# Kernel optimization log

Measured on AMD Instinct MI355X. Metric: run time of the kernel, lower is better.

Reference implementation:

```python
import jax, jax.numpy as jnp
from jax import lax
import numpy as np

B, INP, WIDTH, OUTP, E, H = 32, 1024, 256, 1024, 8, 14
EPS = 1e-5


def setup_inputs() -> dict:
    key = jax.random.key(0)
    ks = jax.random.split(key, 12)
    n = lambda k, s, sc=0.05: jax.random.normal(k, s, jnp.float32) * sc
    return {
        "x": jax.random.normal(ks[0], (B, INP, H, H), jnp.float32),
        "w1": n(ks[1], (E, WIDTH, INP, 1, 1)),
        "w2": n(ks[2], (E, WIDTH, WIDTH, 3, 3)),
        "w3": n(ks[3], (E, OUTP, WIDTH, 1, 1)),
        "r1_w": n(ks[4], (INP, E)), "r1_b": jnp.zeros((E,), jnp.float32),
        "r2_w": n(ks[5], (WIDTH, E)), "r2_b": jnp.zeros((E,), jnp.float32),
        "r3_w": n(ks[6], (WIDTH, E)), "r3_b": jnp.zeros((E,), jnp.float32),
        "bn1_g": jax.random.uniform(ks[7], (WIDTH,), jnp.float32, 0.5, 1.5),
        "bn1_b": n(ks[8], (WIDTH,), 0.1),
        "bn1_m": jnp.zeros((WIDTH,), jnp.float32), "bn1_v": jnp.ones((WIDTH,), jnp.float32),
        "bn2_g": jax.random.uniform(ks[9], (WIDTH,), jnp.float32, 0.5, 1.5),
        "bn2_b": n(ks[10], (WIDTH,), 0.1),
        "bn2_m": jnp.zeros((WIDTH,), jnp.float32), "bn2_v": jnp.ones((WIDTH,), jnp.float32),
        "bn3_g": jax.random.uniform(ks[11], (OUTP,), jnp.float32, 0.5, 1.5),
        "bn3_b": jnp.zeros((OUTP,), jnp.float32),
        "bn3_m": jnp.zeros((OUTP,), jnp.float32), "bn3_v": jnp.ones((OUTP,), jnp.float32),
    }


def _route(x, w, b):
    # global avg pool -> linear -> sigmoid : [B, E]
    return jax.nn.sigmoid(x.mean(axis=(2, 3)) @ w + b)


def _cond_conv(x, w, rw, stride=1, padding=0, dilation=1, groups=1):
    # x: [B,Cin,H,W]; w: [E,Cout,Cin/groups,kh,kw]; rw: [B,E]
    Bn, Cin, Hh, Ww = x.shape
    _, Cout, Cin_g, kh, kw = w.shape
    # per-sample expert-combined kernels, then batch-grouped conv
    cw = jnp.einsum('be,eoikl->boikl', rw, w).reshape(Bn * Cout, Cin_g, kh, kw)
    out = lax.conv_general_dilated(
        x.reshape(1, Bn * Cin, Hh, Ww), cw,
        window_strides=(stride, stride),
        padding=[(padding, padding), (padding, padding)],
        rhs_dilation=(dilation, dilation),
        feature_group_count=Bn * groups,
        dimension_numbers=('NCHW', 'OIHW', 'NCHW'))
    return out.reshape(Bn, Cout, out.shape[2], out.shape[3])


def _bn(x, g, b, m, v):
    inv = lax.rsqrt(v + EPS) * g
    return x * inv[None, :, None, None] + (b - m * inv)[None, :, None, None]


def reference(x, w1, w2, w3, r1_w, r1_b, r2_w, r2_b, r3_w, r3_b,
              bn1_g, bn1_b, bn1_m, bn1_v, bn2_g, bn2_b, bn2_m, bn2_v,
              bn3_g, bn3_b, bn3_m, bn3_v):
    identity = x
    rw1 = _route(x, r1_w, r1_b)
    out = jax.nn.relu(_bn(_cond_conv(x, w1, rw1), bn1_g, bn1_b, bn1_m, bn1_v))
    rw2 = _route(out, r2_w, r2_b)
    out = jax.nn.relu(_bn(_cond_conv(out, w2, rw2, stride=1, padding=1), bn2_g, bn2_b, bn2_m, bn2_v))
    rw3 = _route(out, r3_w, r3_b)
    out = _bn(_cond_conv(out, w3, rw3), bn3_g, bn3_b, bn3_m, bn3_v)
    return jax.nn.relu(out + identity)
```

## Files before the change

### kernel.cpp

```cpp
#include <hip/hip_runtime.h>
#include <hip/hip_bf16.h>

#define BB 32
#define INP 1024
#define WIDTH 256
#define OUTP 1024
#define NE 8
#define HW 196
#define HH 14
#define EPS 1e-5f

#define S1 (WIDTH * INP)
#define S2 (WIDTH * WIDTH * 9)
#define S3 (OUTP * WIDTH)

typedef __attribute__((ext_vector_type(8))) short bf16x8;
typedef __attribute__((ext_vector_type(4))) float f32x4;
typedef __attribute__((ext_vector_type(8))) unsigned short u16x8;


__device__ __forceinline__ unsigned short f2bf_bits(float f) {
    unsigned u = __float_as_uint(f);
    u += 0x7FFFu + ((u >> 16) & 1u);
    return (unsigned short)(u >> 16);
}

#if defined(__has_builtin)
#if __has_builtin(__builtin_amdgcn_global_load_lds)
#define HAVE_GLL 1
#endif
#endif
__device__ __forceinline__ void gl2lds(const unsigned short* g, unsigned short* l,
                                       int lane) {
#ifdef HAVE_GLL
    __builtin_amdgcn_global_load_lds(
        (const __attribute__((address_space(1))) unsigned int*)(const void*)g,
        (__attribute__((address_space(3))) unsigned int*)(void*)l, 16, 0, 0);
#else
    *(u16x8*)(l + lane * 8) = *(const u16x8*)g;
#endif
}

__global__ __launch_bounds__(256) void transpose_mean_x(
    const float* __restrict__ x, unsigned short* __restrict__ xb,
    float* __restrict__ mean1) {
    __shared__ float lt[128][17];
    int b = blockIdx.x, c0 = blockIdx.y * 128;
    int t = threadIdx.x, cr = t >> 1, half = t & 1;
    const float* src = x + ((size_t)(b * INP + c0 + cr)) * HW;
    float msum = 0.f;
    int j = t >> 4, nl = t & 15;
    for (int pg = 0; pg < 14; pg++) {
        int p0 = pg * 16 + half * 8;
        float vv[8];
        if (pg < 12) {
            float4 a = *(const float4*)(src + p0);
            float4 c = *(const float4*)(src + p0 + 4);
            vv[0] = a.x; vv[1] = a.y; vv[2] = a.z; vv[3] = a.w;
            vv[4] = c.x; vv[5] = c.y; vv[6] = c.z; vv[7] = c.w;
        } else {
#pragma unroll
            for (int i = 0; i < 8; i++) {
                int p = p0 + i;
                vv[i] = (p < HW) ? src[p] : 0.f;
            }
        }
#pragma unroll
        for (int i = 0; i < 8; i++) { msum += vv[i]; lt[cr][half * 8 + i] = vv[i]; }
        __syncthreads();
        unsigned short pk[8];
#pragma unroll
        for (int i = 0; i < 8; i++) pk[i] = f2bf_bits(lt[j * 8 + i][nl]);
        size_t tile = ((size_t)b * 14 + pg) * 32 + (size_t)(blockIdx.y * 4 + (j >> 2));
        int lane = nl | ((j & 3) << 4);
        *(u16x8*)(xb + tile * 512 + lane * 8) = *(u16x8*)pk;
        __syncthreads();
    }
    float other = __shfl_xor(msum, 1, 64);
    if (half == 0) mean1[b * INP + c0 + cr] = (msum + other) * (1.0f / (float)HW);
}

__global__ __launch_bounds__(256) void route_kernel(const float* __restrict__ mean,
                                                    const float* __restrict__ W,
                                                    const float* __restrict__ bias,
                                                    float* __restrict__ rw, int C,
                                                    float scale) {
    __shared__ float red[NE * 256];
    int b = blockIdx.x, t = threadIdx.x;
    float part[NE];
#pragma unroll
    for (int e = 0; e < NE; e++) part[e] = 0.f;
    for (int c = t; c < C; c += 256) {
        float m = mean[b * C + c];
#pragma unroll
        for (int e = 0; e < NE; e++) part[e] += m * W[c * NE + e];
    }
#pragma unroll
    for (int e = 0; e < NE; e++) red[e * 256 + t] = part[e];
    __syncthreads();
    for (int st = 128; st > 0; st >>= 1) {
        if (t < st) {
#pragma unroll
            for (int e = 0; e < NE; e++) red[e * 256 + t] += red[e * 256 + t + st];
        }
        __syncthreads();
    }
    if (t < NE) {
        float z = red[t * 256] * scale + bias[t];
        rw[b * NE + t] = 1.0f / (1.0f + expf(-z));
    }
}

__global__ __launch_bounds__(256) void combine_cont(
    const float* __restrict__ w, const float* __restrict__ rw,
    unsigned short* __restrict__ cw, int S, int Mt, int Kt) {
    __shared__ float srw[64];
    int tid = threadIdx.x, wv = tid >> 6, lane = tid & 63, ml = lane & 15, k8l = lane >> 4;
    int g = blockIdx.y;
    if (tid < 64) srw[tid] = rw[g * 64 + tid];
    __syncthreads();
    int kq = Kt >> 2;
    int mt = blockIdx.x / kq, kt = (blockIdx.x - mt * kq) * 4 + wv;
    int K = Kt * 32;
    const float* src = w + (size_t)(mt * 16 + ml) * K + kt * 32 + k8l * 8;
    float v[NE][8];
#pragma unroll
    for (int e = 0; e < NE; e++) {
        float4 a = *(const float4*)(src + (size_t)e * S);
        float4 c = *(const float4*)(src + (size_t)e * S + 4);
        v[e][0] = a.x; v[e][1] = a.y; v[e][2] = a.z; v[e][3] = a.w;
        v[e][4] = c.x; v[e][5] = c.y; v[e][6] = c.z; v[e][7] = c.w;
    }
    size_t dto = ((size_t)mt * Kt + kt) * 512 + (size_t)lane * 8;
    size_t bstr = (size_t)Mt * Kt * 512;
    for (int bl = 0; bl < 8; bl++) {
        int b = g * 8 + bl;
        float acc[8];
#pragma unroll
        for (int jj = 0; jj < 8; jj++) acc[jj] = 0.f;
#pragma unroll
        for (int e = 0; e < NE; e++) {
            float r = srw[bl * NE + e];
#pragma unroll
            for (int jj = 0; jj < 8; jj++) acc[jj] += r * v[e][jj];
        }
        u16x8 o;
#pragma unroll
        for (int jj = 0; jj < 8; jj++) o[jj] = f2bf_bits(acc[jj]);
        *(u16x8*)(cw + (size_t)b * bstr + dto) = o;
    }
}

__global__ __launch_bounds__(256) void permute_w2(
    const float* __restrict__ w2, unsigned short* __restrict__ wb2) {
    __shared__ unsigned short lds[9 * 256];
    int eo = blockIdx.x, t = threadIdx.x;
    const float* src = w2 + (size_t)eo * 2304 + (size_t)t * 9;
#pragma unroll
    for (int t9 = 0; t9 < 9; t9++) lds[t9 * 256 + t] = f2bf_bits(src[t9]);
    __syncthreads();
    unsigned short* dst = wb2 + (size_t)eo * 2304;
    for (int j = t; j < 288; j += 256)
        *(u16x8*)(dst + j * 8) = *(const u16x8*)(lds + j * 8);
}

__global__ __launch_bounds__(256) void combine_w2(
    const unsigned short* __restrict__ wb2, const float* __restrict__ rw,
    unsigned short* __restrict__ cw) {
    __shared__ float srw[64];
    int tid = threadIdx.x, wv = tid >> 6, lane = tid & 63, ol = lane & 15, g4 = lane >> 4;
    int g = blockIdx.y;
    if (tid < 64) srw[tid] = rw[g * 64 + tid];
    __syncthreads();
    int ot = blockIdx.x / 18, kt = (blockIdx.x - ot * 18) * 4 + wv;
    const unsigned short* src = wb2 + (size_t)(ot * 16 + ol) * 2304 + kt * 32 + g4 * 8;
    float v[NE][8];
#pragma unroll
    for (int e = 0; e < NE; e++) {
        u16x8 raw = *(const u16x8*)(src + (size_t)e * S2);
#pragma unroll
        for (int jj = 0; jj < 8; jj++)
            v[e][jj] = __uint_as_float((unsigned)raw[jj] << 16);
    }
    size_t dto = ((size_t)ot * 72 + kt) * 512 + (size_t)lane * 8;
    for (int bl = 0; bl < 8; bl++) {
        int b = g * 8 + bl;
        float acc[8];
#pragma unroll
        for (int jj = 0; jj < 8; jj++) acc[jj] = 0.f;
#pragma unroll
        for (int e = 0; e < NE; e++) {
            float r = srw[bl * NE + e];
#pragma unroll
            for (int jj = 0; jj < 8; jj++) acc[jj] += r * v[e][jj];
        }
        u16x8 out;
#pragma unroll
        for (int jj = 0; jj < 8; jj++) out[jj] = f2bf_bits(acc[jj]);
        *(u16x8*)(cw + (size_t)b * (16 * 72 * 512) + dto) = out;
    }
}

__device__ __forceinline__ void stage_step(
    const unsigned short* Ab, const unsigned short* Bb, int Ktot, int kt,
    unsigned short* lA, unsigned short* lB, int wv, int lane) {
    gl2lds(Ab + ((size_t)wv * Ktot + kt) * 512 + lane * 8, lA + wv * 512, lane);
    gl2lds(Ab + ((size_t)(wv + 4) * Ktot + kt) * 512 + lane * 8, lA + (wv + 4) * 512, lane);
    gl2lds(Bb + ((size_t)wv * Ktot + kt) * 512 + lane * 8, lB + wv * 512, lane);
    if (wv < 3)
        gl2lds(Bb + ((size_t)(4 + wv) * Ktot + kt) * 512 + lane * 8, lB + (4 + wv) * 512, lane);
}

__device__ __forceinline__ void compute_step(
    const unsigned short* lA, const unsigned short* lB,
    f32x4* acc0, f32x4* acc1, int wv, int lane) {
    bf16x8 a0 = *(const bf16x8*)(lA + wv * 512 + lane * 8);
    bf16x8 a1 = *(const bf16x8*)(lA + (wv + 4) * 512 + lane * 8);
#pragma unroll
    for (int t = 0; t < 7; t++) {
        bf16x8 bt = *(const bf16x8*)(lB + t * 512 + lane * 8);
        acc0[t] = __builtin_amdgcn_mfma_f32_16x16x32_bf16(a0, bt, acc0[t], 0, 0, 0);
        acc1[t] = __builtin_amdgcn_mfma_f32_16x16x32_bf16(a1, bt, acc1[t], 0, 0, 0);
    }
}

__global__ __launch_bounds__(256) void gemm_split(
    const unsigned short* __restrict__ Bsw, const unsigned short* __restrict__ Asw,
    float* __restrict__ P, int Ktot, int ksteps) {
    __shared__ __align__(16) unsigned short lAb[4][8 * 512];
    __shared__ __align__(16) unsigned short lBb[4][7 * 512];
    int b = blockIdx.x, mh = blockIdx.y >> 1, nh = blockIdx.y & 1, s = blockIdx.z;
    int tid = threadIdx.x, wv = tid >> 6, lane = tid & 63;
    int kbase = s * ksteps;
    const unsigned short* Ab = Asw + (size_t)(b * 16 + mh * 8) * Ktot * 512;
    const unsigned short* Bb = Bsw + (size_t)(b * 14 + nh * 7) * Ktot * 512;
    f32x4 acc0[7], acc1[7];
#pragma unroll
    for (int t = 0; t < 7; t++) { acc0[t] = {0.f, 0.f, 0.f, 0.f}; acc1[t] = {0.f, 0.f, 0.f, 0.f}; }

    stage_step(Ab, Bb, Ktot, kbase + 0, lAb[0], lBb[0], wv, lane);
    stage_step(Ab, Bb, Ktot, kbase + 1, lAb[1], lBb[1], wv, lane);
    int npair = ksteps >> 1;
    for (int kp = 0; kp < npair; kp++) {
        int cb = (kp & 1) << 1, sb = 2 - cb;
        __syncthreads();
        if (kp + 1 < npair) {
            stage_step(Ab, Bb, Ktot, kbase + 2 * kp + 2, lAb[sb], lBb[sb], wv, lane);
            stage_step(Ab, Bb, Ktot, kbase + 2 * kp + 3, lAb[sb + 1], lBb[sb + 1], wv, lane);
        }
        compute_step(lAb[cb], lBb[cb], acc0, acc1, wv, lane);
        compute_step(lAb[cb + 1], lBb[cb + 1], acc0, acc1, wv, lane);
    }
#pragma unroll
    for (int a = 0; a < 2; a++) {
        int mt = mh * 8 + wv + 4 * a;
#pragma unroll
        for (int t = 0; t < 7; t++) {
            f32x4 v = a ? acc1[t] : acc0[t];
            *(f32x4*)(P + ((((size_t)s * BB + b) * 16 + mt) * 14 + nh * 7 + t) * 256 + lane * 4) = v;
        }
    }
}

__global__ __launch_bounds__(256) void gemm2_split(
    const unsigned short* __restrict__ act, const unsigned short* __restrict__ cw2,
    const unsigned short* __restrict__ zpad, float* __restrict__ P) {
    __shared__ __align__(16) unsigned short lAb[4][8 * 512];
    __shared__ __align__(16) unsigned short lBb[4][7 * 512];
    int b = blockIdx.x, mh = blockIdx.y >> 1, nh = blockIdx.y & 1, s = blockIdx.z;
    int tid = threadIdx.x, wv = tid >> 6, lane = tid & 63, lo = lane & 15, g4 = lane >> 4;
    const unsigned short* Ab = cw2 + (size_t)(b * 16 + mh * 8) * 72 * 512;
    const unsigned short* actb = act + (size_t)b * 14 * 8 * 512;

    int p0 = (nh * 7 + wv) * 16 + lo;
    int py0 = p0 / HH, px0 = p0 - (p0 / HH) * HH;
    bool pv0 = p0 < HW;
    int p1 = (nh * 7 + wv + 4) * 16 + lo;
    int py1 = p1 / HH, px1 = p1 - (p1 / HH) * HH;
    bool pv1 = (wv < 3) && (p1 < HW);

    f32x4 acc0[7], acc1[7];
#pragma unroll
    for (int t = 0; t < 7; t++) { acc0[t] = {0.f, 0.f, 0.f, 0.f}; acc1[t] = {0.f, 0.f, 0.f, 0.f}; }

    int kbase = s * 18;
    auto stage2 = [&](int kt, unsigned short* lA, unsigned short* lB) {
        gl2lds(Ab + ((size_t)wv * 72 + kt) * 512 + lane * 8, lA + wv * 512, lane);
        gl2lds(Ab + ((size_t)(wv + 4) * 72 + kt) * 512 + lane * 8, lA + (wv + 4) * 512, lane);
        int t9 = kt >> 3;
        int dy = t9 / 3 - 1, dx = t9 - (t9 / 3) * 3 - 1;
        int itile = kt & 7;
        {
            int sy = py0 + dy, sx = px0 + dx;
            bool ok = pv0 && sy >= 0 && sy < HH && sx >= 0 && sx < HH;
            int ns = sy * HH + sx;
            const unsigned short* gp = ok
                ? actb + ((size_t)(ns >> 4) * 8 + itile) * 512 + (size_t)((ns & 15) | (g4 << 4)) * 8
                : zpad;
            gl2lds(gp, lB + wv * 512, lane);
        }
        if (wv < 3) {
            int sy = py1 + dy, sx = px1 + dx;
            bool ok = pv1 && sy >= 0 && sy < HH && sx >= 0 && sx < HH;
            int ns = sy * HH + sx;
            const unsigned short* gp = ok
                ? actb + ((size_t)(ns >> 4) * 8 + itile) * 512 + (size_t)((ns & 15) | (g4 << 4)) * 8
                : zpad;
            gl2lds(gp, lB + (wv + 4) * 512, lane);
        }
    };

    stage2(kbase + 0, lAb[0], lBb[0]);
    stage2(kbase + 1, lAb[1], lBb[1]);
    for (int kp = 0; kp < 9; kp++) {
        int cb = (kp & 1) << 1, sb = 2 - cb;
        __syncthreads();
        if (kp < 8) {
            stage2(kbase + 2 * kp + 2, lAb[sb], lBb[sb]);
            stage2(kbase + 2 * kp + 3, lAb[sb + 1], lBb[sb + 1]);
        }
        compute_step(lAb[cb], lBb[cb], acc0, acc1, wv, lane);
        compute_step(lAb[cb + 1], lBb[cb + 1], acc0, acc1, wv, lane);
    }
#pragma unroll
    for (int a = 0; a < 2; a++) {
        int mt = mh * 8 + wv + 4 * a;
#pragma unroll
        for (int t = 0; t < 7; t++) {
            f32x4 v = a ? acc1[t] : acc0[t];
            *(f32x4*)(P + ((((size_t)s * BB + b) * 16 + mt) * 14 + nh * 7 + t) * 256 + lane * 4) = v;
        }
    }
}

__global__ __launch_bounds__(256) void ep12(
    const float* __restrict__ P, int S,
    const float* __restrict__ g, const float* __restrict__ be,
    const float* __restrict__ mu, const float* __restrict__ var,
    unsigned short* __restrict__ actout, float* __restrict__ msum) {
    int b = blockIdx.x;
    int tid = threadIdx.x, wv = tid >> 6, lane = tid & 63, lo = lane & 15, g4 = lane >> 4;
    int mt = blockIdx.y * 4 + wv;
    int nt0 = blockIdx.z * 7;
    int c0 = mt * 16 + g4 * 4;
    float sc[4], sh[4];
#pragma unroll
    for (int r = 0; r < 4; r++) {
        float iv = rsqrtf(var[c0 + r] + EPS) * g[c0 + r];
        sc[r] = iv;
        sh[r] = be[c0 + r] - mu[c0 + r] * iv;
    }
    const float* Pb = P + (((size_t)b * 16 + mt) * 14) * 256 + lane * 4;
    size_t pstr = (size_t)BB * 16 * 14 * 256;
    float ms[4] = {0.f, 0.f, 0.f, 0.f};
    int ktc = mt >> 1;
    int lanehi = ((mt * 2 + (g4 >> 1)) & 3) << 4;
    for (int nt = nt0; nt < nt0 + 7; nt++) {
        float v[4] = {0.f, 0.f, 0.f, 0.f};
        for (int s = 0; s < S; s++) {
            f32x4 pv = *(const f32x4*)(Pb + (size_t)s * pstr + (size_t)nt * 256);
#pragma unroll
            for (int r = 0; r < 4; r++) v[r] += pv[r];
        }
        int n = nt * 16 + lo;
#pragma unroll
        for (int r = 0; r < 4; r++) {
            float val = v[r] * sc[r] + sh[r];
            val = fmaxf(val, 0.f);
            if (n >= HW) val = 0.f;
            v[r] = val;
            ms[r] += val;
        }
        unsigned p01 = (unsigned)f2bf_bits(v[0]) | ((unsigned)f2bf_bits(v[1]) << 16);
        unsigned p23 = (unsigned)f2bf_bits(v[2]) | ((unsigned)f2bf_bits(v[3]) << 16);
        size_t off = (((size_t)(b * 14 + nt)) * 8 + ktc) * 512 + (size_t)(lo | lanehi) * 8 + (g4 & 1) * 4;
        *(uint2*)(actout + off) = make_uint2(p01, p23);
    }
#pragma unroll
    for (int r = 0; r < 4; r++) {
        float s = ms[r];
        s += __shfl_xor(s, 1, 64);
        s += __shfl_xor(s, 2, 64);
        s += __shfl_xor(s, 4, 64);
        s += __shfl_xor(s, 8, 64);
        if (lo == 0) atomicAdd(&msum[b * 256 + c0 + r], s);
    }
}

__global__ __launch_bounds__(256) void gemm3_fused(
    const unsigned short* __restrict__ Bsw, const unsigned short* __restrict__ Asw,
    const float* __restrict__ g, const float* __restrict__ be,
    const float* __restrict__ mu, const float* __restrict__ var,
    const float* __restrict__ resid, float* __restrict__ out) {
    __shared__ __align__(16) unsigned short lAb[4][8 * 512];
    __shared__ __align__(16) unsigned short lBb[4][7 * 512];
    int b = blockIdx.x, y = blockIdx.y, mh = y >> 1, nh = y & 1;
    int tid = threadIdx.x, wv = tid >> 6, lane = tid & 63, lo = lane & 15, g4 = lane >> 4;
    const unsigned short* Ab = Asw + (size_t)(b * 64 + mh * 8) * 8 * 512;
    const unsigned short* Bb = Bsw + (size_t)(b * 14 + nh * 7) * 8 * 512;
    f32x4 acc0[7], acc1[7];
#pragma unroll
    for (int t = 0; t < 7; t++) { acc0[t] = {0.f, 0.f, 0.f, 0.f}; acc1[t] = {0.f, 0.f, 0.f, 0.f}; }

    stage_step(Ab, Bb, 8, 0, lAb[0], lBb[0], wv, lane);
    stage_step(Ab, Bb, 8, 1, lAb[1], lBb[1], wv, lane);
#pragma unroll
    for (int kp = 0; kp < 4; kp++) {
        int cb = (kp & 1) << 1, sb = 2 - cb;
        __syncthreads();
        if (kp + 1 < 4) {
            stage_step(Ab, Bb, 8, 2 * kp + 2, lAb[sb], lBb[sb], wv, lane);
            stage_step(Ab, Bb, 8, 2 * kp + 3, lAb[sb + 1], lBb[sb + 1], wv, lane);
        }
        compute_step(lAb[cb], lBb[cb], acc0, acc1, wv, lane);
        compute_step(lAb[cb + 1], lBb[cb + 1], acc0, acc1, wv, lane);
    }
#pragma unroll
    for (int a = 0; a < 2; a++) {
        int mt = mh * 8 + wv + 4 * a;
        int c0 = mt * 16 + g4 * 4;
        float sc[4], sh[4];
#pragma unroll
        for (int r = 0; r < 4; r++) {
            float iv = rsqrtf(var[c0 + r] + EPS) * g[c0 + r];
            sc[r] = iv;
            sh[r] = be[c0 + r] - mu[c0 + r] * iv;
        }
#pragma unroll
        for (int t = 0; t < 7; t++) {
            int n = (nh * 7 + t) * 16 + lo;
            if (n >= HW) continue;
            f32x4 av = a ? acc1[t] : acc0[t];
#pragma unroll
            for (int r = 0; r < 4; r++) {
                size_t oidx = ((size_t)(b * OUTP + c0 + r)) * HW + n;
                float val = av[r] * sc[r] + sh[r] + resid[oidx];
                out[oidx] = fmaxf(val, 0.f);
            }
        }
    }
}

extern "C" void kernel_launch(void* const* d_in, const int* in_sizes, int n_in,
                              void* d_out, int out_size, void* d_ws, size_t ws_size,
                              hipStream_t stream) {
    const float* x    = (const float*)d_in[0];
    const float* w1   = (const float*)d_in[1];
    const float* w2   = (const float*)d_in[2];
    const float* w3   = (const float*)d_in[3];
    const float* r1_w = (const float*)d_in[4];
    const float* r1_b = (const float*)d_in[5];
    const float* r2_w = (const float*)d_in[6];
    const float* r2_b = (const float*)d_in[7];
    const float* r3_w = (const float*)d_in[8];
    const float* r3_b = (const float*)d_in[9];
    const float* bn1_g = (const float*)d_in[10];
    const float* bn1_b = (const float*)d_in[11];
    const float* bn1_m = (const float*)d_in[12];
    const float* bn1_v = (const float*)d_in[13];
    const float* bn2_g = (const float*)d_in[14];
    const float* bn2_b = (const float*)d_in[15];
    const float* bn2_m = (const float*)d_in[16];
    const float* bn2_v = (const float*)d_in[17];
    const float* bn3_g = (const float*)d_in[18];
    const float* bn3_b = (const float*)d_in[19];
    const float* bn3_m = (const float*)d_in[20];
    const float* bn3_v = (const float*)d_in[21];
    float* out = (float*)d_out;

    char* ws = (char*)d_ws;
    size_t off = 0;
    float* mean1 = (float*)(ws + off); off += (size_t)BB * INP * 4;
    float* msum2 = (float*)(ws + off); off += (size_t)BB * 256 * 4;
    float* msum3 = (float*)(ws + off); off += (size_t)BB * 256 * 4;
    float* rw1 = (float*)(ws + off); off += BB * NE * 4;
    float* rw2 = (float*)(ws + off); off += BB * NE * 4;
    float* rw3 = (float*)(ws + off); off += BB * NE * 4;
    unsigned short* zpad = (unsigned short*)(ws + off); off += 256;
    off = (off + 255) & ~(size_t)255;
    unsigned short* act = (unsigned short*)(ws + off); off += (size_t)BB * 14 * 8 * 512 * 2;
    char* cw2slot = ws + off; off += (size_t)BB * 16 * 72 * 512 * 2;
    float* P1           = (float*)cw2slot;
    unsigned short* cw2 = (unsigned short*)cw2slot;
    char* regionA = ws + off; off += (size_t)BB * (14 + 16) * 32 * 512 * 2;
    unsigned short* xb  = (unsigned short*)regionA;
    unsigned short* cw1 = (unsigned short*)(regionA + (size_t)BB * 14 * 32 * 512 * 2);
    unsigned short* wb2 = (unsigned short*)regionA;
    float* P2           = (float*)regionA;
    unsigned short* cw3 = (unsigned short*)regionA;
    (void)ws_size;

    hipMemsetAsync(zpad, 0, 256, stream);
    hipMemsetAsync(msum2, 0, (size_t)2 * BB * 256 * 4, stream);
    transpose_mean_x<<<dim3(BB, 8), 256, 0, stream>>>(x, xb, mean1);

    route_kernel<<<BB, 256, 0, stream>>>(mean1, r1_w, r1_b, rw1, INP, 1.0f);
    combine_cont<<<dim3(128, 4), 256, 0, stream>>>(w1, rw1, cw1, S1, 16, 32);
    gemm_split<<<dim3(BB, 4, 4), 256, 0, stream>>>(xb, cw1, P1, 32, 8);
    permute_w2<<<2048, 256, 0, stream>>>(w2, wb2);
    ep12<<<dim3(BB, 4, 2), 256, 0, stream>>>(P1, 4, bn1_g, bn1_b, bn1_m, bn1_v, act, msum2);

    route_kernel<<<BB, 256, 0, stream>>>(msum2, r2_w, r2_b, rw2, WIDTH, 1.0f / (float)HW);
    combine_w2<<<dim3(288, 4), 256, 0, stream>>>(wb2, rw2, cw2);
    gemm2_split<<<dim3(BB, 4, 4), 256, 0, stream>>>(act, cw2, zpad, P2);
    ep12<<<dim3(BB, 4, 2), 256, 0, stream>>>(P2, 4, bn2_g, bn2_b, bn2_m, bn2_v, act, msum3);

    route_kernel<<<BB, 256, 0, stream>>>(msum3, r3_w, r3_b, rw3, WIDTH, 1.0f / (float)HW);
    combine_cont<<<dim3(128, 4), 256, 0, stream>>>(w3, rw3, cw3, S3, 64, 8);
    gemm3_fused<<<dim3(BB, 16), 256, 0, stream>>>(act, cw3, bn3_g, bn3_b, bn3_m, bn3_v, x, out);
}
```

Baseline: 261.4 us.

## Fuse routing into combine kernels and replace split-K GEMMs with fused epilogues

```diff
diff --git a/kernel.cpp b/kernel.cpp
--- a/kernel.cpp
+++ b/kernel.cpp
@@ -39,6 +39,43 @@
 #else
     *(u16x8*)(l + lane * 8) = *(const u16x8*)g;
 #endif
+}
+
+__device__ __forceinline__ void block_route(
+    const float* __restrict__ vec, const float* __restrict__ W,
+    const float* __restrict__ bias, float scale, int C, int g,
+    float* srw, int tid) {
+    int wv = tid >> 6, lane = tid & 63;
+    float p0[NE], p1[NE];
+#pragma unroll
+    for (int e = 0; e < NE; e++) { p0[e] = 0.f; p1[e] = 0.f; }
+    const float* v0 = vec + (size_t)(g * 8 + wv * 2) * C;
+    const float* v1 = v0 + C;
+    for (int c = lane; c < C; c += 64) {
+        float4 wa = *(const float4*)(W + c * 8);
+        float4 wb = *(const float4*)(W + c * 8 + 4);
+        float m0 = v0[c], m1 = v1[c];
+        p0[0] += m0 * wa.x; p0[1] += m0 * wa.y; p0[2] += m0 * wa.z; p0[3] += m0 * wa.w;
+        p0[4] += m0 * wb.x; p0[5] += m0 * wb.y; p0[6] += m0 * wb.z; p0[7] += m0 * wb.w;
+        p1[0] += m1 * wa.x; p1[1] += m1 * wa.y; p1[2] += m1 * wa.z; p1[3] += m1 * wa.w;
+        p1[4] += m1 * wb.x; p1[5] += m1 * wb.y; p1[6] += m1 * wb.z; p1[7] += m1 * wb.w;
+    }
+#pragma unroll
+    for (int j = 1; j < 64; j <<= 1) {
+#pragma unroll
+        for (int e = 0; e < NE; e++) {
+            p0[e] += __shfl_xor(p0[e], j, 64);
+            p1[e] += __shfl_xor(p1[e], j, 64);
+        }
+    }
+    if (lane == 0) {
+#pragma unroll
+        for (int e = 0; e < NE; e++) {
+            srw[(wv * 2) * 8 + e] = 1.0f / (1.0f + expf(-(scale * p0[e] + bias[e])));
+            srw[(wv * 2 + 1) * 8 + e] = 1.0f / (1.0f + expf(-(scale * p1[e] + bias[e])));
+        }
+    }
+    __syncthreads();
 }
 
 __global__ __launch_bounds__(256) void transpose_mean_x(
@@ -80,45 +117,14 @@
     if (half == 0) mean1[b * INP + c0 + cr] = (msum + other) * (1.0f / (float)HW);
 }
 
-__global__ __launch_bounds__(256) void route_kernel(const float* __restrict__ mean,
-                                                    const float* __restrict__ W,
-                                                    const float* __restrict__ bias,
-                                                    float* __restrict__ rw, int C,
-                                                    float scale) {
-    __shared__ float red[NE * 256];
-    int b = blockIdx.x, t = threadIdx.x;
-    float part[NE];
-#pragma unroll
-    for (int e = 0; e < NE; e++) part[e] = 0.f;
-    for (int c = t; c < C; c += 256) {
-        float m = mean[b * C + c];
-#pragma unroll
-        for (int e = 0; e < NE; e++) part[e] += m * W[c * NE + e];
-    }
-#pragma unroll
-    for (int e = 0; e < NE; e++) red[e * 256 + t] = part[e];
-    __syncthreads();
-    for (int st = 128; st > 0; st >>= 1) {
-        if (t < st) {
-#pragma unroll
-            for (int e = 0; e < NE; e++) red[e * 256 + t] += red[e * 256 + t + st];
-        }
-        __syncthreads();
-    }
-    if (t < NE) {
-        float z = red[t * 256] * scale + bias[t];
-        rw[b * NE + t] = 1.0f / (1.0f + expf(-z));
-    }
-}
-
-__global__ __launch_bounds__(256) void combine_cont(
-    const float* __restrict__ w, const float* __restrict__ rw,
+__global__ __launch_bounds__(256) void combine_cont_r(
+    const float* __restrict__ w, const float* __restrict__ vec,
+    const float* __restrict__ rW, const float* __restrict__ rB, float scale, int C,
     unsigned short* __restrict__ cw, int S, int Mt, int Kt) {
     __shared__ float srw[64];
     int tid = threadIdx.x, wv = tid >> 6, lane = tid & 63, ml = lane & 15, k8l = lane >> 4;
     int g = blockIdx.y;
-    if (tid < 64) srw[tid] = rw[g * 64 + tid];
-    __syncthreads();
+    block_route(vec, rW, rB, scale, C, g, srw, tid);
     int kq = Kt >> 2;
     int mt = blockIdx.x / kq, kt = (blockIdx.x - mt * kq) * 4 + wv;
     int K = Kt * 32;
@@ -164,14 +170,14 @@
         *(u16x8*)(dst + j * 8) = *(const u16x8*)(lds + j * 8);
 }
 
-__global__ __launch_bounds__(256) void combine_w2(
-    const unsigned short* __restrict__ wb2, const float* __restrict__ rw,
+__global__ __launch_bounds__(256) void combine_w2_r(
+    const unsigned short* __restrict__ wb2, const float* __restrict__ vec,
+    const float* __restrict__ rW, const float* __restrict__ rB, float scale,
     unsigned short* __restrict__ cw) {
     __shared__ float srw[64];
     int tid = threadIdx.x, wv = tid >> 6, lane = tid & 63, ol = lane & 15, g4 = lane >> 4;
     int g = blockIdx.y;
-    if (tid < 64) srw[tid] = rw[g * 64 + tid];
-    __syncthreads();
+    block_route(vec, rW, rB, scale, 256, g, srw, tid);
     int ot = blockIdx.x / 18, kt = (blockIdx.x - ot * 18) * 4 + wv;
     const unsigned short* src = wb2 + (size_t)(ot * 16 + ol) * 2304 + kt * 32 + g4 * 8;
     float v[NE][8];
@@ -201,75 +207,108 @@
     }
 }
 
-__device__ __forceinline__ void stage_step(
-    const unsigned short* Ab, const unsigned short* Bb, int Ktot, int kt,
-    unsigned short* lA, unsigned short* lB, int wv, int lane) {
-    gl2lds(Ab + ((size_t)wv * Ktot + kt) * 512 + lane * 8, lA + wv * 512, lane);
-    gl2lds(Ab + ((size_t)(wv + 4) * Ktot + kt) * 512 + lane * 8, lA + (wv + 4) * 512, lane);
-    gl2lds(Bb + ((size_t)wv * Ktot + kt) * 512 + lane * 8, lB + wv * 512, lane);
-    if (wv < 3)
-        gl2lds(Bb + ((size_t)(4 + wv) * Ktot + kt) * 512 + lane * 8, lB + (4 + wv) * 512, lane);
-}
-
-__device__ __forceinline__ void compute_step(
-    const unsigned short* lA, const unsigned short* lB,
-    f32x4* acc0, f32x4* acc1, int wv, int lane) {
-    bf16x8 a0 = *(const bf16x8*)(lA + wv * 512 + lane * 8);
-    bf16x8 a1 = *(const bf16x8*)(lA + (wv + 4) * 512 + lane * 8);
+__device__ __forceinline__ void epilogue_act(
+    const f32x4* acc, int b, int mt, int nh, int lo, int g4,
+    const float* __restrict__ g, const float* __restrict__ be,
+    const float* __restrict__ mu, const float* __restrict__ var,
+    unsigned short* __restrict__ actout, float* __restrict__ msum) {
+    int c0 = mt * 16 + g4 * 4;
+    float sc[4], sh[4];
+#pragma unroll
+    for (int r = 0; r < 4; r++) {
+        float iv = rsqrtf(var[c0 + r] + EPS) * g[c0 + r];
+        sc[r] = iv;
+        sh[r] = be[c0 + r] - mu[c0 + r] * iv;
+    }
+    float ms[4] = {0.f, 0.f, 0.f, 0.f};
+    int ktc = mt >> 1;
+    int lanehi = ((mt * 2 + (g4 >> 1)) & 3) << 4;
 #pragma unroll
     for (int t = 0; t < 7; t++) {
-        bf16x8 bt = *(const bf16x8*)(lB + t * 512 + lane * 8);
-        acc0[t] = __builtin_amdgcn_mfma_f32_16x16x32_bf16(a0, bt, acc0[t], 0, 0, 0);
-        acc1[t] = __builtin_amdgcn_mfma_f32_16x16x32_bf16(a1, bt, acc1[t], 0, 0, 0);
-    }
-}
-
-__global__ __launch_bounds__(256) void gemm_split(
+        int nt = nh * 7 + t;
+        int n = nt * 16 + lo;
+        float v[4];
+#pragma unroll
+        for (int r = 0; r < 4; r++) {
+            float val = acc[t][r] * sc[r] + sh[r];
+            val = fmaxf(val, 0.f);
+            if (n >= HW) val = 0.f;
+            v[r] = val;
+            ms[r] += val;
+        }
+        unsigned p01 = (unsigned)f2bf_bits(v[0]) | ((unsigned)f2bf_bits(v[1]) << 16);
+        unsigned p23 = (unsigned)f2bf_bits(v[2]) | ((unsigned)f2bf_bits(v[3]) << 16);
+        size_t off = (((size_t)(b * 14 + nt)) * 8 + ktc) * 512 + (size_t)(lo | lanehi) * 8 + (g4 & 1) * 4;
+        *(uint2*)(actout + off) = make_uint2(p01, p23);
+    }
+#pragma unroll
+    for (int r = 0; r < 4; r++) {
+        float s = ms[r];
+        s += __shfl_xor(s, 1, 64);
+        s += __shfl_xor(s, 2, 64);
+        s += __shfl_xor(s, 4, 64);
+        s += __shfl_xor(s, 8, 64);
+        if (lo == 0) atomicAdd(&msum[b * 256 + c0 + r], s);
+    }
+}
+
+__global__ __launch_bounds__(256) void gemm1_fused(
     const unsigned short* __restrict__ Bsw, const unsigned short* __restrict__ Asw,
-    float* __restrict__ P, int Ktot, int ksteps) {
-    __shared__ __align__(16) unsigned short lAb[4][8 * 512];
+    const float* __restrict__ g, const float* __restrict__ be,
+    const float* __restrict__ mu, const float* __restrict__ var,
+    unsigned short* __restrict__ actout, float* __restrict__ msum) {
+    __shared__ __align__(16) unsigned short lAb[4][4 * 512];
     __shared__ __align__(16) unsigned short lBb[4][7 * 512];
-    int b = blockIdx.x, mh = blockIdx.y >> 1, nh = blockIdx.y & 1, s = blockIdx.z;
-    int tid = threadIdx.x, wv = tid >> 6, lane = tid & 63;
-    int kbase = s * ksteps;
-    const unsigned short* Ab = Asw + (size_t)(b * 16 + mh * 8) * Ktot * 512;
-    const unsigned short* Bb = Bsw + (size_t)(b * 14 + nh * 7) * Ktot * 512;
-    f32x4 acc0[7], acc1[7];
-#pragma unroll
-    for (int t = 0; t < 7; t++) { acc0[t] = {0.f, 0.f, 0.f, 0.f}; acc1[t] = {0.f, 0.f, 0.f, 0.f}; }
-
-    stage_step(Ab, Bb, Ktot, kbase + 0, lAb[0], lBb[0], wv, lane);
-    stage_step(Ab, Bb, Ktot, kbase + 1, lAb[1], lBb[1], wv, lane);
-    int npair = ksteps >> 1;
-    for (int kp = 0; kp < npair; kp++) {
+    const int Kt = 32;
+    int b = blockIdx.x, mh = blockIdx.y, nh = blockIdx.z;
+    int tid = threadIdx.x, wv = tid >> 6, lane = tid & 63, lo = lane & 15, g4 = lane >> 4;
+    const unsigned short* Ab = Asw + (size_t)(b * 16 + mh * 4) * Kt * 512;
+    const unsigned short* Bb = Bsw + (size_t)(b * 14 + nh * 7) * Kt * 512;
+    f32x4 acc[7];
+#pragma unroll
+    for (int t = 0; t < 7; t++) acc[t] = {0.f, 0.f, 0.f, 0.f};
+
+    auto stage = [&](int kt, unsigned short* lA, unsigned short* lB) {
+        gl2lds(Ab + ((size_t)wv * Kt + kt) * 512 + lane * 8, lA + wv * 512, lane);
+        gl2lds(Bb + ((size_t)wv * Kt + kt) * 512 + lane * 8, lB + wv * 512, lane);
+        if (wv < 3)
+            gl2lds(Bb + ((size_t)(4 + wv) * Kt + kt) * 512 + lane * 8, lB + (4 + wv) * 512, lane);
+    };
+    auto compute = [&](const unsigned short* lA, const unsigned short* lB) {
+        bf16x8 a0 = *(const bf16x8*)(lA + wv * 512 + lane * 8);
+#pragma unroll
+        for (int t = 0; t < 7; t++) {
+            bf16x8 bt = *(const bf16x8*)(lB + t * 512 + lane * 8);
+            acc[t] = __builtin_amdgcn_mfma_f32_16x16x32_bf16(a0, bt, acc[t], 0, 0, 0);
+        }
+    };
+
+    stage(0, lAb[0], lBb[0]);
+    stage(1, lAb[1], lBb[1]);
+    for (int kp = 0; kp < 16; kp++) {
         int cb = (kp & 1) << 1, sb = 2 - cb;
         __syncthreads();
-        if (kp + 1 < npair) {
-            stage_step(Ab, Bb, Ktot, kbase + 2 * kp + 2, lAb[sb], lBb[sb], wv, lane);
-            stage_step(Ab, Bb, Ktot, kbase + 2 * kp + 3, lAb[sb + 1], lBb[sb + 1], wv, lane);
-        }
-        compute_step(lAb[cb], lBb[cb], acc0, acc1, wv, lane);
-        compute_step(lAb[cb + 1], lBb[cb + 1], acc0, acc1, wv, lane);
-    }
-#pragma unroll
-    for (int a = 0; a < 2; a++) {
-        int mt = mh * 8 + wv + 4 * a;
-#pragma unroll
-        for (int t = 0; t < 7; t++) {
-            f32x4 v = a ? acc1[t] : acc0[t];
-            *(f32x4*)(P + ((((size_t)s * BB + b) * 16 + mt) * 14 + nh * 7 + t) * 256 + lane * 4) = v;
-        }
-    }
-}
-
-__global__ __launch_bounds__(256) void gemm2_split(
+        if (kp < 15) {
+            stage(2 * kp + 2, lAb[sb], lBb[sb]);
+            stage(2 * kp + 3, lAb[sb + 1], lBb[sb + 1]);
+        }
+        compute(lAb[cb], lBb[cb]);
+        compute(lAb[cb + 1], lBb[cb + 1]);
+    }
+    epilogue_act(acc, b, mh * 4 + wv, nh, lo, g4, g, be, mu, var, actout, msum);
+}
+
+__global__ __launch_bounds__(256) void gemm2_fused(
     const unsigned short* __restrict__ act, const unsigned short* __restrict__ cw2,
-    const unsigned short* __restrict__ zpad, float* __restrict__ P) {
-    __shared__ __align__(16) unsigned short lAb[4][8 * 512];
+    const unsigned short* __restrict__ zpad,
+    const float* __restrict__ g, const float* __restrict__ be,
+    const float* __restrict__ mu, const float* __restrict__ var,
+    unsigned short* __restrict__ actout, float* __restrict__ msum) {
+    __shared__ __align__(16) unsigned short lAb[4][4 * 512];
     __shared__ __align__(16) unsigned short lBb[4][7 * 512];
-    int b = blockIdx.x, mh = blockIdx.y >> 1, nh = blockIdx.y & 1, s = blockIdx.z;
+    int b = blockIdx.x, mh = blockIdx.y, nh = blockIdx.z;
     int tid = threadIdx.x, wv = tid >> 6, lane = tid & 63, lo = lane & 15, g4 = lane >> 4;
-    const unsigned short* Ab = cw2 + (size_t)(b * 16 + mh * 8) * 72 * 512;
+    const unsigned short* Ab = cw2 + (size_t)(b * 16 + mh * 4) * 72 * 512;
     const unsigned short* actb = act + (size_t)b * 14 * 8 * 512;
 
     int p0 = (nh * 7 + wv) * 16 + lo;
@@ -279,14 +318,12 @@
     int py1 = p1 / HH, px1 = p1 - (p1 / HH) * HH;
     bool pv1 = (wv < 3) && (p1 < HW);
 
-    f32x4 acc0[7], acc1[7];
-#pragma unroll
-    for (int t = 0; t < 7; t++) { acc0[t] = {0.f, 0.f, 0.f, 0.f}; acc1[t] = {0.f, 0.f, 0.f, 0.f}; }
-
-    int kbase = s * 18;
-    auto stage2 = [&](int kt, unsigned short* lA, unsigned short* lB) {
+    f32x4 acc[7];
+#pragma unroll
+    for (int t = 0; t < 7; t++) acc[t] = {0.f, 0.f, 0.f, 0.f};
+
+    auto stage = [&](int kt, unsigned short* lA, unsigned short* lB) {
         gl2lds(Ab + ((size_t)wv * 72 + kt) * 512 + lane * 8, lA + wv * 512, lane);
-        gl2lds(Ab + ((size_t)(wv + 4) * 72 + kt) * 512 + lane * 8, lA + (wv + 4) * 512, lane);
         int t9 = kt >> 3;
         int dy = t9 / 3 - 1, dx = t9 - (t9 / 3) * 3 - 1;
         int itile = kt & 7;
@@ -309,82 +346,28 @@
             gl2lds(gp, lB + (wv + 4) * 512, lane);
         }
     };
-
-    stage2(kbase + 0, lAb[0], lBb[0]);
-    stage2(kbase + 1, lAb[1], lBb[1]);
-    for (int kp = 0; kp < 9; kp++) {
+    auto compute = [&](const unsigned short* lA, const unsigned short* lB) {
+        bf16x8 a0 = *(const bf16x8*)(lA + wv * 512 + lane * 8);
+#pragma unroll
+        for (int t = 0; t < 7; t++) {
+            bf16x8 bt = *(const bf16x8*)(lB + t * 512 + lane * 8);
+            acc[t] = __builtin_amdgcn_mfma_f32_16x16x32_bf16(a0, bt, acc[t], 0, 0, 0);
+        }
+    };
+
+    stage(0, lAb[0], lBb[0]);
+    stage(1, lAb[1], lBb[1]);
+    for (int kp = 0; kp < 36; kp++) {
         int cb = (kp & 1) << 1, sb = 2 - cb;
         __syncthreads();
-        if (kp < 8) {
-            stage2(kbase + 2 * kp + 2, lAb[sb], lBb[sb]);
-            stage2(kbase + 2 * kp + 3, lAb[sb + 1], lBb[sb + 1]);
-        }
-        compute_step(lAb[cb], lBb[cb], acc0, acc1, wv, lane);
-        compute_step(lAb[cb + 1], lBb[cb + 1], acc0, acc1, wv, lane);
-    }
-#pragma unroll
-    for (int a = 0; a < 2; a++) {
-        int mt = mh * 8 + wv + 4 * a;
-#pragma unroll
-        for (int t = 0; t < 7; t++) {
-            f32x4 v = a ? acc1[t] : acc0[t];
-            *(f32x4*)(P + ((((size_t)s * BB + b) * 16 + mt) * 14 + nh * 7 + t) * 256 + lane * 4) = v;
-        }
-    }
-}
-
-__global__ __launch_bounds__(256) void ep12(
-    const float* __restrict__ P, int S,
-    const float* __restrict__ g, const float* __restrict__ be,
-    const float* __restrict__ mu, const float* __restrict__ var,
-    unsigned short* __restrict__ actout, float* __restrict__ msum) {
-    int b = blockIdx.x;
-    int tid = threadIdx.x, wv = tid >> 6, lane = tid & 63, lo = lane & 15, g4 = lane >> 4;
-    int mt = blockIdx.y * 4 + wv;
-    int nt0 = blockIdx.z * 7;
-    int c0 = mt * 16 + g4 * 4;
-    float sc[4], sh[4];
-#pragma unroll
-    for (int r = 0; r < 4; r++) {
-        float iv = rsqrtf(var[c0 + r] + EPS) * g[c0 + r];
-        sc[r] = iv;
-        sh[r] = be[c0 + r] - mu[c0 + r] * iv;
-    }
-    const float* Pb = P + (((size_t)b * 16 + mt) * 14) * 256 + lane * 4;
-    size_t pstr = (size_t)BB * 16 * 14 * 256;
-    float ms[4] = {0.f, 0.f, 0.f, 0.f};
-    int ktc = mt >> 1;
-    int lanehi = ((mt * 2 + (g4 >> 1)) & 3) << 4;
-    for (int nt = nt0; nt < nt0 + 7; nt++) {
-        float v[4] = {0.f, 0.f, 0.f, 0.f};
-        for (int s = 0; s < S; s++) {
-            f32x4 pv = *(const f32x4*)(Pb + (size_t)s * pstr + (size_t)nt * 256);
-#pragma unroll
-            for (int r = 0; r < 4; r++) v[r] += pv[r];
-        }
-        int n = nt * 16 + lo;
-#pragma unroll
-        for (int r = 0; r < 4; r++) {
-            float val = v[r] * sc[r] + sh[r];
-            val = fmaxf(val, 0.f);
-            if (n >= HW) val = 0.f;
-            v[r] = val;
-            ms[r] += val;
-        }
-        unsigned p01 = (unsigned)f2bf_bits(v[0]) | ((unsigned)f2bf_bits(v[1]) << 16);
-        unsigned p23 = (unsigned)f2bf_bits(v[2]) | ((unsigned)f2bf_bits(v[3]) << 16);
-        size_t off = (((size_t)(b * 14 + nt)) * 8 + ktc) * 512 + (size_t)(lo | lanehi) * 8 + (g4 & 1) * 4;
-        *(uint2*)(actout + off) = make_uint2(p01, p23);
-    }
-#pragma unroll
-    for (int r = 0; r < 4; r++) {
-        float s = ms[r];
-        s += __shfl_xor(s, 1, 64);
-        s += __shfl_xor(s, 2, 64);
-        s += __shfl_xor(s, 4, 64);
-        s += __shfl_xor(s, 8, 64);
-        if (lo == 0) atomicAdd(&msum[b * 256 + c0 + r], s);
-    }
+        if (kp < 35) {
+            stage(2 * kp + 2, lAb[sb], lBb[sb]);
+            stage(2 * kp + 3, lAb[sb + 1], lBb[sb + 1]);
+        }
+        compute(lAb[cb], lBb[cb]);
+        compute(lAb[cb + 1], lBb[cb + 1]);
+    }
+    epilogue_act(acc, b, mh * 4 + wv, nh, lo, g4, g, be, mu, var, actout, msum);
 }
 
 __global__ __launch_bounds__(256) void gemm3_fused(
@@ -402,18 +385,36 @@
 #pragma unroll
     for (int t = 0; t < 7; t++) { acc0[t] = {0.f, 0.f, 0.f, 0.f}; acc1[t] = {0.f, 0.f, 0.f, 0.f}; }
 
-    stage_step(Ab, Bb, 8, 0, lAb[0], lBb[0], wv, lane);
-    stage_step(Ab, Bb, 8, 1, lAb[1], lBb[1], wv, lane);
+    auto stage = [&](int kt, unsigned short* lA, unsigned short* lB) {
+        gl2lds(Ab + ((size_t)wv * 8 + kt) * 512 + lane * 8, lA + wv * 512, lane);
+        gl2lds(Ab + ((size_t)(wv + 4) * 8 + kt) * 512 + lane * 8, lA + (wv + 4) * 512, lane);
+        gl2lds(Bb + ((size_t)wv * 8 + kt) * 512 + lane * 8, lB + wv * 512, lane);
+        if (wv < 3)
+            gl2lds(Bb + ((size_t)(4 + wv) * 8 + kt) * 512 + lane * 8, lB + (4 + wv) * 512, lane);
+    };
+    auto compute = [&](const unsigned short* lA, const unsigned short* lB) {
+        bf16x8 a0 = *(const bf16x8*)(lA + wv * 512 + lane * 8);
+        bf16x8 a1 = *(const bf16x8*)(lA + (wv + 4) * 512 + lane * 8);
+#pragma unroll
+        for (int t = 0; t < 7; t++) {
+            bf16x8 bt = *(const bf16x8*)(lB + t * 512 + lane * 8);
+            acc0[t] = __builtin_amdgcn_mfma_f32_16x16x32_bf16(a0, bt, acc0[t], 0, 0, 0);
+            acc1[t] = __builtin_amdgcn_mfma_f32_16x16x32_bf16(a1, bt, acc1[t], 0, 0, 0);
+        }
+    };
+
+    stage(0, lAb[0], lBb[0]);
+    stage(1, lAb[1], lBb[1]);
 #pragma unroll
     for (int kp = 0; kp < 4; kp++) {
         int cb = (kp & 1) << 1, sb = 2 - cb;
         __syncthreads();
         if (kp + 1 < 4) {
-            stage_step(Ab, Bb, 8, 2 * kp + 2, lAb[sb], lBb[sb], wv, lane);
-            stage_step(Ab, Bb, 8, 2 * kp + 3, lAb[sb + 1], lBb[sb + 1], wv, lane);
-        }
-        compute_step(lAb[cb], lBb[cb], acc0, acc1, wv, lane);
-        compute_step(lAb[cb + 1], lBb[cb + 1], acc0, acc1, wv, lane);
+            stage(2 * kp + 2, lAb[sb], lBb[sb]);
+            stage(2 * kp + 3, lAb[sb + 1], lBb[sb + 1]);
+        }
+        compute(lAb[cb], lBb[cb]);
+        compute(lAb[cb + 1], lBb[cb + 1]);
     }
 #pragma unroll
     for (int a = 0; a < 2; a++) {
@@ -473,39 +474,35 @@
     float* mean1 = (float*)(ws + off); off += (size_t)BB * INP * 4;
     float* msum2 = (float*)(ws + off); off += (size_t)BB * 256 * 4;
     float* msum3 = (float*)(ws + off); off += (size_t)BB * 256 * 4;
-    float* rw1 = (float*)(ws + off); off += BB * NE * 4;
-    float* rw2 = (float*)(ws + off); off += BB * NE * 4;
-    float* rw3 = (float*)(ws + off); off += BB * NE * 4;
     unsigned short* zpad = (unsigned short*)(ws + off); off += 256;
     off = (off + 255) & ~(size_t)255;
-    unsigned short* act = (unsigned short*)(ws + off); off += (size_t)BB * 14 * 8 * 512 * 2;
-    char* cw2slot = ws + off; off += (size_t)BB * 16 * 72 * 512 * 2;
-    float* P1           = (float*)cw2slot;
-    unsigned short* cw2 = (unsigned short*)cw2slot;
+    unsigned short* act1 = (unsigned short*)(ws + off); off += (size_t)BB * 14 * 8 * 512 * 2;
+    unsigned short* act2 = (unsigned short*)(ws + off); off += (size_t)BB * 14 * 8 * 512 * 2;
+    unsigned short* cw2 = (unsigned short*)(ws + off); off += (size_t)BB * 16 * 72 * 512 * 2;
     char* regionA = ws + off; off += (size_t)BB * (14 + 16) * 32 * 512 * 2;
     unsigned short* xb  = (unsigned short*)regionA;
     unsigned short* cw1 = (unsigned short*)(regionA + (size_t)BB * 14 * 32 * 512 * 2);
     unsigned short* wb2 = (unsigned short*)regionA;
-    float* P2           = (float*)regionA;
     unsigned short* cw3 = (unsigned short*)regionA;
     (void)ws_size;
 
-    hipMemsetAsync(zpad, 0, 256, stream);
-    hipMemsetAsync(msum2, 0, (size_t)2 * BB * 256 * 4, stream);
+    hipMemsetAsync(msum2, 0, (size_t)2 * BB * 256 * 4 + 256, stream);
     transpose_mean_x<<<dim3(BB, 8), 256, 0, stream>>>(x, xb, mean1);
 
-    route_kernel<<<BB, 256, 0, stream>>>(mean1, r1_w, r1_b, rw1, INP, 1.0f);
-    combine_cont<<<dim3(128, 4), 256, 0, stream>>>(w1, rw1, cw1, S1, 16, 32);
-    gemm_split<<<dim3(BB, 4, 4), 256, 0, stream>>>(xb, cw1, P1, 32, 8);
+    combine_cont_r<<<dim3(128, 4), 256, 0, stream>>>(w1, mean1, r1_w, r1_b, 1.0f, INP,
+                                                     cw1, S1, 16, 32);
+    gemm1_fused<<<dim3(BB, 4, 2), 256, 0, stream>>>(xb, cw1, bn1_g, bn1_b, bn1_m, bn1_v,
+                                                    act1, msum2);
     permute_w2<<<2048, 256, 0, stream>>>(w2, wb2);
-    ep12<<<dim3(BB, 4, 2), 256, 0, stream>>>(P1, 4, bn1_g, bn1_b, bn1_m, bn1_v, act, msum2);
-
-    route_kernel<<<BB, 256, 0, stream>>>(msum2, r2_w, r2_b, rw2, WIDTH, 1.0f / (float)HW);
-    combine_w2<<<dim3(288, 4), 256, 0, stream>>>(wb2, rw2, cw2);
-    gemm2_split<<<dim3(BB, 4, 4), 256, 0, stream>>>(act, cw2, zpad, P2);
-    ep12<<<dim3(BB, 4, 2), 256, 0, stream>>>(P2, 4, bn2_g, bn2_b, bn2_m, bn2_v, act, msum3);
-
-    route_kernel<<<BB, 256, 0, stream>>>(msum3, r3_w, r3_b, rw3, WIDTH, 1.0f / (float)HW);
-    combine_cont<<<dim3(128, 4), 256, 0, stream>>>(w3, rw3, cw3, S3, 64, 8);
-    gemm3_fused<<<dim3(BB, 16), 256, 0, stream>>>(act, cw3, bn3_g, bn3_b, bn3_m, bn3_v, x, out);
-}
+
+    combine_w2_r<<<dim3(288, 4), 256, 0, stream>>>(wb2, msum2, r2_w, r2_b,
+                                                   1.0f / (float)HW, cw2);
+    gemm2_fused<<<dim3(BB, 4, 2), 256, 0, stream>>>(act1, cw2, zpad, bn2_g, bn2_b,
+                                                    bn2_m, bn2_v, act2, msum3);
+
+    combine_cont_r<<<dim3(128, 4), 256, 0, stream>>>(w3, msum3, r3_w, r3_b,
+                                                     1.0f / (float)HW, WIDTH,
+                                                     cw3, S3, 64, 8);
+    gemm3_fused<<<dim3(BB, 16), 256, 0, stream>>>(act2, cw3, bn3_g, bn3_b, bn3_m, bn3_v,
+                                                  x, out);
+}
```

Result: faster. 254.6 us (-2.6%).
